# Kernel optimization log

Measured on AMD Instinct MI355X. Metric: run time of the kernel, lower is better.

The kernel has to match this reference:

```python
import jax, jax.numpy as jnp
import numpy as np

ALPHA = 4.0          # spikingjelly default surrogate.Sigmoid(alpha=4.0)
V_TH = 1.0           # IFNode default v_threshold
BN_EPS = 1e-5

@jax.custom_vjp
def spike(x):
    # heaviside forward
    return (x >= 0.0).astype(x.dtype)

def _spike_fwd(x):
    return spike(x), x

def _spike_bwd(x, g):
    s = jax.nn.sigmoid(ALPHA * x)
    return (g * ALPHA * s * (1.0 - s),)

spike.defvjp(_spike_fwd, _spike_bwd)

def if_node(x_seq):
    """Multi-step IF neuron: integrate, threshold, hard reset (v_reset=0),
    detach_reset=True. x_seq: [T, ...] -> spikes [T, ...]."""
    def step(v, xt):
        v = v + xt
        s = spike(v - V_TH)
        v = v * (1.0 - jax.lax.stop_gradient(s))  # detached hard reset to 0
        return v, s
    _, s_seq = jax.lax.scan(step, jnp.zeros_like(x_seq[0]), x_seq)
    return s_seq

def bn1d(x, gamma, beta):
    """Training-mode BatchNorm1d over flattened (T*B) batch dim. x: [T,B,F]."""
    m = x.mean(axis=(0, 1))
    v = x.var(axis=(0, 1))  # biased variance, matches torch normalization
    return (x - m) * jax.lax.rsqrt(v + BN_EPS) * gamma + beta

def setup_inputs() -> dict:
    key = jax.random.key(0)
    ks = jax.random.split(key, 12)
    T, B, C, H, W = 8, 64, 2, 128, 128
    F0, D, NC = C * H * W, 2048, 1000
    x = jax.random.uniform(ks[0], (T, B, C, H, W), dtype=jnp.float32)
    def kaiming(k, out_f, in_f):
        # kaiming_normal_ mode='fan_out', relu gain: std = sqrt(2/out_f)
        return jax.random.normal(k, (out_f, in_f), dtype=jnp.float32) * np.sqrt(2.0 / out_f)
    def bias(k, out_f, in_f):
        bound = 1.0 / np.sqrt(in_f)
        return jax.random.uniform(k, (out_f,), dtype=jnp.float32, minval=-bound, maxval=bound)
    inp = {"x": x}
    dims = [(D, F0), (D, D), (D, D)]
    for i, (o, f) in enumerate(dims):
        inp[f"W{i}"] = kaiming(ks[1 + i], o, f)
        inp[f"b{i}"] = bias(ks[4 + i], o, f)
        inp[f"g{i}"] = jnp.ones((o,), jnp.float32)
        inp[f"be{i}"] = jnp.zeros((o,), jnp.float32)
    inp["Wout"] = kaiming(ks[7], NC, D)
    inp["bout"] = bias(ks[8], NC, D)
    return inp

def reference(x, W0, b0, g0, be0, W1, b1, g1, be1, W2, b2, g2, be2, Wout, bout):
    T, B = x.shape[0], x.shape[1]
    h = x.reshape(T, B, -1)           # [T,B,32768]
    h = if_node(h)                    # sn0
    for Wl, bl, gl, bel in ((W0, b0, g0, be0), (W1, b1, g1, be1), (W2, b2, g2, be2)):
        h = jnp.einsum('tbi,oi->tbo', h, Wl) + bl
        h = bn1d(h, gl, bel)
        h = if_node(h)
    out = jnp.einsum('tbi,oi->tbo', h, Wout) + bout  # [T,B,1000]
    return out.mean(axis=0)           # [B,1000]
```

## Files before the change

kernel.cpp:

```cpp
#include <hip/hip_runtime.h>


#define T_STEPS 8
#define BATCH 64
#define F0 32768
#define DIM 2048
#define NROWS 512
#define NC 1000

typedef __attribute__((ext_vector_type(8))) short short8;
typedef __attribute__((ext_vector_type(4))) float f32x4;

__device__ __forceinline__ unsigned short bf16_rne(float f) {
    unsigned int u = __float_as_uint(f);
    u += 0x7FFFu + ((u >> 16) & 1u);
    return (unsigned short)(u >> 16);
}

#define BM 128
#define BN 128
#define BK 64

__device__ __forceinline__ short8 lds_frag(const unsigned short* base, int row, int kb) {
    const int off = row * 128 + (kb ^ ((row & 7) << 4));
    return *(const short8*)((const char*)base + off);
}

__global__ __launch_bounds__(512) void gemm_splitk(
    const unsigned short* __restrict__ A, const float* __restrict__ W,
    float* __restrict__ part, int M, int N, int K, int Kpart, int Wrows)
{
    __shared__ unsigned short As[BM * BK];
    __shared__ unsigned short Hs[BN * BK];
    __shared__ unsigned short Ls[BN * BK];

    const int gx = gridDim.x, gy = gridDim.y;
    const int nwg = gx * gy * gridDim.z;
    const int lid = blockIdx.x + gx * (blockIdx.y + gy * blockIdx.z);
    const int cpx = nwg >> 3;
    const int nid = (lid & 7) * cpx + (lid >> 3);
    const int bx  = nid % gx;
    const int by  = (nid / gx) % gy;
    const int kz  = nid / (gx * gy);

    const int tid  = threadIdx.x;
    const int lane = tid & 63;
    const int w    = tid >> 6;
    const int bm   = bx * BM;
    const int bn   = by * BN;
    const int ksteps = Kpart / BK;
    const int wm = (w >> 2) * 64;
    const int wn = (w & 3) * 32;

    f32x4 acc[4][2] = {};

    for (int kt = 0; kt < ksteps; ++kt) {
        const int k0 = kz * Kpart + kt * BK;

#pragma unroll
        for (int c = 0; c < 2; ++c) {
            const int r    = w * 16 + c * 8 + (lane >> 3);
            const int colb = ((lane & 7) * 16) ^ ((r & 7) << 4);
            const char* src = (const char*)A + ((size_t)(bm + r) * K + k0) * 2 + colb;
            unsigned short* dst = &As[(w * 16 + c * 8) * BK];
            __builtin_amdgcn_global_load_lds(
                (const __attribute__((address_space(1))) void*)src,
                (__attribute__((address_space(3))) void*)dst, 16, 0, 0);
        }

        float4 wv[4];
#pragma unroll
        for (int i = 0; i < 4; ++i) {
            const int q  = tid + 512 * i;
            const int n  = q >> 4;
            const int c4 = q & 15;
            const int gn = min(bn + n, Wrows - 1);
            wv[i] = *(const float4*)&W[(size_t)gn * K + k0 + c4 * 4];
        }
#pragma unroll
        for (int i = 0; i < 4; ++i) {
            const int q  = tid + 512 * i;
            const int n  = q >> 4;
            const int c4 = q & 15;
            const float vf[4] = {wv[i].x, wv[i].y, wv[i].z, wv[i].w};
            unsigned short h[4], l[4];
#pragma unroll
            for (int e = 0; e < 4; ++e) {
                h[e] = bf16_rne(vf[e]);
                const float hf = __uint_as_float((unsigned int)h[e] << 16);
                l[e] = bf16_rne(vf[e] - hf);
            }
            const int off = n * 128 + ((c4 * 8) ^ ((n & 7) << 4));
            *(ushort4*)((char*)Hs + off) = make_ushort4(h[0], h[1], h[2], h[3]);
            *(ushort4*)((char*)Ls + off) = make_ushort4(l[0], l[1], l[2], l[3]);
        }

        __syncthreads();

#pragma unroll
        for (int kk = 0; kk < 2; ++kk) {
            const int kb = (kk * 32 + (lane >> 4) * 8) * 2;
            short8 a[4], bh[2], bl[2];
#pragma unroll
            for (int i = 0; i < 4; ++i)
                a[i] = lds_frag(As, wm + i * 16 + (lane & 15), kb);
#pragma unroll
            for (int i = 0; i < 2; ++i) {
                const int r = wn + i * 16 + (lane & 15);
                bh[i] = lds_frag(Hs, r, kb);
                bl[i] = lds_frag(Ls, r, kb);
            }
#pragma unroll
            for (int mi = 0; mi < 4; ++mi)
#pragma unroll
                for (int ni = 0; ni < 2; ++ni) {
                    acc[mi][ni] = __builtin_amdgcn_mfma_f32_16x16x32_bf16(
                        a[mi], bh[ni], acc[mi][ni], 0, 0, 0);
                    acc[mi][ni] = __builtin_amdgcn_mfma_f32_16x16x32_bf16(
                        a[mi], bl[ni], acc[mi][ni], 0, 0, 0);
                }
        }
        __syncthreads();
    }

    const size_t zoff = (size_t)kz * M * N;
#pragma unroll
    for (int mi = 0; mi < 4; ++mi) {
        const int gr0 = bm + wm + mi * 16 + (lane >> 4) * 4;
#pragma unroll
        for (int ni = 0; ni < 2; ++ni) {
            const int gc = bn + wn + ni * 16 + (lane & 15);
            if (gc < N) {
#pragma unroll
                for (int e = 0; e < 4; ++e) {
                    const int gr = gr0 + e;
                    if (gr < M) part[zoff + (size_t)gr * N + gc] = acc[mi][ni][e];
                }
            }
        }
    }
}

__global__ __launch_bounds__(256) void reduce_bias(
    const float* __restrict__ part, const float* __restrict__ bias,
    float* __restrict__ out, int KS, int MN, int N)
{
    const int i4 = blockIdx.x * 256 + threadIdx.x;
    if (i4 * 4 >= MN) return;
    float4 s = make_float4(0.f, 0.f, 0.f, 0.f);
    for (int z = 0; z < KS; ++z) {
        const float4 p = *(const float4*)&part[(size_t)z * MN + i4 * 4];
        s.x += p.x; s.y += p.y; s.z += p.z; s.w += p.w;
    }
    const int col = (i4 * 4) % N;
    const float4 b = *(const float4*)&bias[col];
    s.x += b.x; s.y += b.y; s.z += b.z; s.w += b.w;
    *(float4*)&out[(size_t)i4 * 4] = s;
}

__global__ __launch_bounds__(256) void if0_kernel(
    const float* __restrict__ x, unsigned short* __restrict__ s)
{
    const size_t id4 = ((size_t)blockIdx.x * 256 + threadIdx.x) * 4;
    float v0 = 0.f, v1 = 0.f, v2 = 0.f, v3 = 0.f;
#pragma unroll
    for (int t = 0; t < T_STEPS; ++t) {
        const size_t idx = (size_t)t * (BATCH * (size_t)F0) + id4;
        const float4 xv = *(const float4*)&x[idx];
        ushort4 o;
        v0 += xv.x; if (v0 >= 1.f) { o.x = 0x3F80; v0 = 0.f; } else o.x = 0;
        v1 += xv.y; if (v1 >= 1.f) { o.y = 0x3F80; v1 = 0.f; } else o.y = 0;
        v2 += xv.z; if (v2 >= 1.f) { o.z = 0x3F80; v2 = 0.f; } else o.z = 0;
        v3 += xv.w; if (v3 >= 1.f) { o.w = 0x3F80; v3 = 0.f; } else o.w = 0;
        *(ushort4*)&s[idx] = o;
    }
}

__global__ __launch_bounds__(256) void bn_stats_if(
    const float* __restrict__ z, const float* __restrict__ g,
    const float* __restrict__ be, unsigned short* __restrict__ s)
{
    __shared__ float ssum[4][64], ssq[4][64];
    __shared__ float ssc[64], ssh[64];
    const int l = threadIdx.x & 63;
    const int q = threadIdx.x >> 6;
    const int f = blockIdx.x * 64 + l;
    float sum = 0.f, sq = 0.f;
    for (int r = q; r < NROWS; r += 4) {
        const float v = z[(size_t)r * DIM + f];
        sum += v; sq += v * v;
    }
    ssum[q][l] = sum; ssq[q][l] = sq;
    __syncthreads();
    if (threadIdx.x < 64) {
        float ts = 0.f, tq = 0.f;
#pragma unroll
        for (int i = 0; i < 4; ++i) { ts += ssum[i][l]; tq += ssq[i][l]; }
        const float mean = ts * (1.0f / NROWS);
        const float var  = tq * (1.0f / NROWS) - mean * mean;
        const float inv  = rsqrtf(var + 1e-5f);
        const float sc   = g[f] * inv;
        ssc[l] = sc;
        ssh[l] = be[f] - mean * sc;
    }
    __syncthreads();
    const float sc = ssc[l];
    const float sh = ssh[l];
    for (int b = q; b < BATCH; b += 4) {
        const int id = b * DIM + f;
        float v = 0.f;
#pragma unroll
        for (int t = 0; t < T_STEPS; ++t) {
            const size_t idx = (size_t)t * (BATCH * DIM) + id;
            v += z[idx] * sc + sh;
            if (v >= 1.0f) { s[idx] = 0x3F80; v = 0.f; }
            else           { s[idx] = 0; }
        }
    }
}

__global__ __launch_bounds__(256) void bn_stats_if_mean(
    const float* __restrict__ z, const float* __restrict__ g,
    const float* __restrict__ be, unsigned short* __restrict__ sbar)
{
    __shared__ float ssum[4][64], ssq[4][64];
    __shared__ float ssc[64], ssh[64];
    const int l = threadIdx.x & 63;
    const int q = threadIdx.x >> 6;
    const int f = blockIdx.x * 64 + l;
    float sum = 0.f, sq = 0.f;
    for (int r = q; r < NROWS; r += 4) {
        const float v = z[(size_t)r * DIM + f];
        sum += v; sq += v * v;
    }
    ssum[q][l] = sum; ssq[q][l] = sq;
    __syncthreads();
    if (threadIdx.x < 64) {
        float ts = 0.f, tq = 0.f;
#pragma unroll
        for (int i = 0; i < 4; ++i) { ts += ssum[i][l]; tq += ssq[i][l]; }
        const float mean = ts * (1.0f / NROWS);
        const float var  = tq * (1.0f / NROWS) - mean * mean;
        const float inv  = rsqrtf(var + 1e-5f);
        const float sc   = g[f] * inv;
        ssc[l] = sc;
        ssh[l] = be[f] - mean * sc;
    }
    __syncthreads();
    const float sc = ssc[l];
    const float sh = ssh[l];
    for (int b = q; b < BATCH; b += 4) {
        const int id = b * DIM + f;
        float v = 0.f;
        int cnt = 0;
#pragma unroll
        for (int t = 0; t < T_STEPS; ++t) {
            const size_t idx = (size_t)t * (BATCH * DIM) + id;
            v += z[idx] * sc + sh;
            if (v >= 1.0f) { cnt++; v = 0.f; }
        }
        sbar[id] = bf16_rne((float)cnt * 0.125f);
    }
}

extern "C" void kernel_launch(void* const* d_in, const int* in_sizes, int n_in,
                              void* d_out, int out_size, void* d_ws, size_t ws_size,
                              hipStream_t stream)
{
    const float* x    = (const float*)d_in[0];
    const float* W0   = (const float*)d_in[1];
    const float* b0   = (const float*)d_in[2];
    const float* g0   = (const float*)d_in[3];
    const float* be0  = (const float*)d_in[4];
    const float* W1   = (const float*)d_in[5];
    const float* b1   = (const float*)d_in[6];
    const float* g1   = (const float*)d_in[7];
    const float* be1  = (const float*)d_in[8];
    const float* W2   = (const float*)d_in[9];
    const float* b2   = (const float*)d_in[10];
    const float* g2   = (const float*)d_in[11];
    const float* be2  = (const float*)d_in[12];
    const float* Wout = (const float*)d_in[13];
    const float* bout = (const float*)d_in[14];
    float* out = (float*)d_out;
    (void)in_sizes; (void)n_in; (void)out_size; (void)ws_size;

    char* ws = (char*)d_ws;
    size_t off = 0;
    auto alloc = [&](size_t nbytes) {
        char* p = ws + off;
        off = (off + nbytes + 255) & ~(size_t)255;
        return p;
    };
    unsigned short* s0 = (unsigned short*)alloc((size_t)NROWS * F0 * 2);
    unsigned short* s1 = (unsigned short*)alloc((size_t)NROWS * DIM * 2);
    unsigned short* s2 = (unsigned short*)alloc((size_t)NROWS * DIM * 2);
    unsigned short* sb = (unsigned short*)alloc((size_t)128 * DIM * 2);
    float* z    = (float*)alloc((size_t)NROWS * DIM * 4);
    float* part = (float*)alloc((size_t)16 * NROWS * DIM * 4);

    const int MN = NROWS * DIM;

    if0_kernel<<<(BATCH * (size_t)F0) / 4 / 256, 256, 0, stream>>>(x, s0);

    gemm_splitk<<<dim3(NROWS / BM, DIM / BN, 16), 512, 0, stream>>>(
        s0, W0, part, NROWS, DIM, F0, F0 / 16, DIM);
    reduce_bias<<<MN / 4 / 256, 256, 0, stream>>>(part, b0, z, 16, MN, DIM);
    bn_stats_if<<<DIM / 64, 256, 0, stream>>>(z, g0, be0, s1);

    gemm_splitk<<<dim3(NROWS / BM, DIM / BN, 8), 512, 0, stream>>>(
        s1, W1, part, NROWS, DIM, DIM, DIM / 8, DIM);
    reduce_bias<<<MN / 4 / 256, 256, 0, stream>>>(part, b1, z, 8, MN, DIM);
    bn_stats_if<<<DIM / 64, 256, 0, stream>>>(z, g1, be1, s2);

    gemm_splitk<<<dim3(NROWS / BM, DIM / BN, 8), 512, 0, stream>>>(
        s2, W2, part, NROWS, DIM, DIM, DIM / 8, DIM);
    reduce_bias<<<MN / 4 / 256, 256, 0, stream>>>(part, b2, z, 8, MN, DIM);
    bn_stats_if_mean<<<DIM / 64, 256, 0, stream>>>(z, g2, be2, sb);

    gemm_splitk<<<dim3(1, (NC + BN - 1) / BN, 4), 512, 0, stream>>>(
        sb, Wout, part, BATCH, NC, DIM, DIM / 4, NC);
    reduce_bias<<<(BATCH * NC / 4 + 255) / 256, 256, 0, stream>>>(
        part, bout, out, 4, BATCH * NC, NC);
}
```

Baseline: 400.1 us.

## Double-buffer A tile and prefetch next W slice in split-K GEMM

```diff
diff --git a/kernel.cpp b/kernel.cpp
--- a/kernel.cpp
+++ b/kernel.cpp
@@ -21,6 +21,10 @@
 #define BN 128
 #define BK 64
 
+#define SBAR() do { __builtin_amdgcn_sched_barrier(0); \
+                    __builtin_amdgcn_s_barrier();      \
+                    __builtin_amdgcn_sched_barrier(0); } while (0)
+
 __device__ __forceinline__ short8 lds_frag(const unsigned short* base, int row, int kb) {
     const int off = row * 128 + (kb ^ ((row & 7) << 4));
     return *(const short8*)((const char*)base + off);
@@ -30,7 +34,7 @@
     const unsigned short* __restrict__ A, const float* __restrict__ W,
     float* __restrict__ part, int M, int N, int K, int Kpart, int Wrows)
 {
-    __shared__ unsigned short As[BM * BK];
+    __shared__ unsigned short As[2][BM * BK];
     __shared__ unsigned short Hs[BN * BK];
     __shared__ unsigned short Ls[BN * BK];
 
@@ -51,37 +55,37 @@
     const int ksteps = Kpart / BK;
     const int wm = (w >> 2) * 64;
     const int wn = (w & 3) * 32;
+    const int kbase = kz * Kpart;
 
     f32x4 acc[4][2] = {};
-
-    for (int kt = 0; kt < ksteps; ++kt) {
-        const int k0 = kz * Kpart + kt * BK;
-
+    float4 wv[4];
+
+    auto issue_loads = [&](int buf, int kt) {
+        const int k0 = kbase + kt * BK;
+#pragma unroll
+        for (int i = 0; i < 4; ++i) {
+            const int n  = (tid >> 4) + 32 * i;
+            const int c4 = tid & 15;
+            const int gn = min(bn + n, Wrows - 1);
+            wv[i] = *(const float4*)&W[(size_t)gn * K + k0 + c4 * 4];
+        }
 #pragma unroll
         for (int c = 0; c < 2; ++c) {
             const int r    = w * 16 + c * 8 + (lane >> 3);
             const int colb = ((lane & 7) * 16) ^ ((r & 7) << 4);
             const char* src = (const char*)A + ((size_t)(bm + r) * K + k0) * 2 + colb;
-            unsigned short* dst = &As[(w * 16 + c * 8) * BK];
+            unsigned short* dst = &As[buf][(w * 16 + c * 8) * BK];
             __builtin_amdgcn_global_load_lds(
                 (const __attribute__((address_space(1))) void*)src,
                 (__attribute__((address_space(3))) void*)dst, 16, 0, 0);
         }
-
-        float4 wv[4];
+    };
+
+    auto convert_write = [&]() {
 #pragma unroll
         for (int i = 0; i < 4; ++i) {
-            const int q  = tid + 512 * i;
-            const int n  = q >> 4;
-            const int c4 = q & 15;
-            const int gn = min(bn + n, Wrows - 1);
-            wv[i] = *(const float4*)&W[(size_t)gn * K + k0 + c4 * 4];
-        }
-#pragma unroll
-        for (int i = 0; i < 4; ++i) {
-            const int q  = tid + 512 * i;
-            const int n  = q >> 4;
-            const int c4 = q & 15;
+            const int n  = (tid >> 4) + 32 * i;
+            const int c4 = tid & 15;
             const float vf[4] = {wv[i].x, wv[i].y, wv[i].z, wv[i].w};
             unsigned short h[4], l[4];
 #pragma unroll
@@ -94,8 +98,17 @@
             *(ushort4*)((char*)Hs + off) = make_ushort4(h[0], h[1], h[2], h[3]);
             *(ushort4*)((char*)Ls + off) = make_ushort4(l[0], l[1], l[2], l[3]);
         }
-
-        __syncthreads();
+    };
+
+    issue_loads(0, 0);
+    convert_write();
+    asm volatile("s_waitcnt vmcnt(0) lgkmcnt(0)" ::: "memory");
+    SBAR();
+
+    int cur = 0;
+    for (int kt = 0; kt < ksteps; ++kt) {
+        const bool last = (kt + 1 == ksteps);
+        if (!last) issue_loads(cur ^ 1, kt + 1);
 
 #pragma unroll
         for (int kk = 0; kk < 2; ++kk) {
@@ -103,7 +116,7 @@
             short8 a[4], bh[2], bl[2];
 #pragma unroll
             for (int i = 0; i < 4; ++i)
-                a[i] = lds_frag(As, wm + i * 16 + (lane & 15), kb);
+                a[i] = lds_frag(&As[cur][0], wm + i * 16 + (lane & 15), kb);
 #pragma unroll
             for (int i = 0; i < 2; ++i) {
                 const int r = wn + i * 16 + (lane & 15);
@@ -120,7 +133,14 @@
                         a[mi], bl[ni], acc[mi][ni], 0, 0, 0);
                 }
         }
-        __syncthreads();
+
+        if (!last) {
+            SBAR();
+            convert_write();
+            asm volatile("s_waitcnt vmcnt(0) lgkmcnt(0)" ::: "memory");
+            SBAR();
+            cur ^= 1;
+        }
     }
 
     const size_t zoff = (size_t)kz * M * N;
@@ -303,9 +323,9 @@
 
     if0_kernel<<<(BATCH * (size_t)F0) / 4 / 256, 256, 0, stream>>>(x, s0);
 
-    gemm_splitk<<<dim3(NROWS / BM, DIM / BN, 16), 512, 0, stream>>>(
-        s0, W0, part, NROWS, DIM, F0, F0 / 16, DIM);
-    reduce_bias<<<MN / 4 / 256, 256, 0, stream>>>(part, b0, z, 16, MN, DIM);
+    gemm_splitk<<<dim3(NROWS / BM, DIM / BN, 8), 512, 0, stream>>>(
+        s0, W0, part, NROWS, DIM, F0, F0 / 8, DIM);
+    reduce_bias<<<MN / 4 / 256, 256, 0, stream>>>(part, b0, z, 8, MN, DIM);
     bn_stats_if<<<DIM / 64, 256, 0, stream>>>(z, g0, be0, s1);
 
     gemm_splitk<<<dim3(NROWS / BM, DIM / BN, 8), 512, 0, stream>>>(
@@ -318,8 +338,8 @@
     reduce_bias<<<MN / 4 / 256, 256, 0, stream>>>(part, b2, z, 8, MN, DIM);
     bn_stats_if_mean<<<DIM / 64, 256, 0, stream>>>(z, g2, be2, sb);
 
-    gemm_splitk<<<dim3(1, (NC + BN - 1) / BN, 4), 512, 0, stream>>>(
-        sb, Wout, part, BATCH, NC, DIM, DIM / 4, NC);
+    gemm_splitk<<<dim3(1, (NC + BN - 1) / BN, 8), 512, 0, stream>>>(
+        sb, Wout, part, BATCH, NC, DIM, DIM / 8, NC);
     reduce_bias<<<(BATCH * NC / 4 + 255) / 256, 256, 0, stream>>>(
-        part, bout, out, 4, BATCH * NC, NC);
-}
+        part, bout, out, 8, BATCH * NC, NC);
+}
```

New measurement: 395.1 us. Within noise of the previous version (-1.3%).
